# Kernel tuning notes

Measured on AMD Instinct MI355X. Metric: run time of the kernel, lower is better.

The kernel has to match this reference:

```python
import jax, jax.numpy as jnp
import numpy as np

N = 8192
IN_F = 256
OUT_F = 256
ALPHA = 0.2  # LeakyReLU negative slope
NEG_INF = -1e12


def setup_inputs() -> dict:
    key = jax.random.key(0)
    k1, k2, k3, k4, k5 = jax.random.split(key, 5)
    inp = jax.random.normal(k1, (N, IN_F), dtype=jnp.float32)
    adj = jax.random.randint(k2, (N, N), 0, 2, dtype=jnp.int32)
    # xavier_uniform with gain=1.414
    def xavier(k, shape, gain=1.414):
        fan_in, fan_out = shape[0], shape[1]
        bound = gain * np.sqrt(6.0 / (fan_in + fan_out))
        return jax.random.uniform(k, shape, jnp.float32, -bound, bound)
    W = xavier(k3, (IN_F, OUT_F))
    a = xavier(k4, (2 * OUT_F, 1))
    wtrans = xavier(k5, (2 * IN_F, OUT_F))
    return {"inp": inp, "adj": adj, "W": W, "a": a, "wtrans": wtrans}


def reference(inp, adj, W, a, wtrans):
    h = inp @ W                                  # [N, OUT_F]
    Wh1 = h @ a[:OUT_F, :]                       # [N, 1]
    Wh2 = h @ a[OUT_F:, :]                       # [N, 1]
    e = jax.nn.leaky_relu(Wh1 + Wh2.T, ALPHA)    # [N, N]
    mask = adj > 0
    attention = jax.nn.softmax(jnp.where(mask, e, NEG_INF), axis=1)
    negative_attention = -jax.nn.softmax(jnp.where(mask, -e, NEG_INF), axis=1)
    # dropout=0.0 / eval mode -> identity
    h_prime = attention @ inp                    # [N, IN_F]
    h_prime_negative = negative_attention @ inp  # [N, IN_F]
    h_prime_double = jnp.concatenate([h_prime, h_prime_negative], axis=1)
    new_h_prime = h_prime_double @ wtrans        # [N, OUT_F]
    return jax.nn.elu(new_h_prime)               # concat=True
```

## Files before the change

kernel.cpp:

```cpp
#include <hip/hip_runtime.h>
#include <stdint.h>

#define GN 8192

typedef float f32x4 __attribute__((ext_vector_type(4)));
typedef short s16x8 __attribute__((ext_vector_type(8)));
typedef unsigned short u16x8 __attribute__((ext_vector_type(8)));

__device__ __forceinline__ unsigned short f2bf(float f) {
    unsigned int u = __float_as_uint(f);
    u += 0x7FFFu + ((u >> 16) & 1u);
    return (unsigned short)(u >> 16);
}
__device__ __forceinline__ float bf2f(unsigned short h) {
    return __uint_as_float(((unsigned int)h) << 16);
}

__global__ void kA(const float* __restrict__ W, const float* __restrict__ a,
                   float* __restrict__ w1, float* __restrict__ w2) {
    int k = blockIdx.x, l = threadIdx.x;
    float s1 = 0.f, s2 = 0.f;
#pragma unroll
    for (int q = 0; q < 4; ++q) {
        int o = l + q * 64;
        float w = W[k * 256 + o];
        s1 += w * a[o];
        s2 += w * a[256 + o];
    }
#pragma unroll
    for (int off = 32; off; off >>= 1) {
        s1 += __shfl_xor(s1, off);
        s2 += __shfl_xor(s2, off);
    }
    if (l == 0) {
        w1[k] = s1;
        w2[k] = s2;
    }
}

__global__ void kA2(const float* __restrict__ wt, unsigned short* __restrict__ wtT) {
    int k = blockIdx.x;
    int o = threadIdx.x;
    wtT[(size_t)o * 512 + k] = f2bf(wt[(size_t)k * 256 + o]);
}

__global__ __launch_bounds__(256) void kB(const float* __restrict__ inp,
                                          const float* __restrict__ w1,
                                          const float* __restrict__ w2,
                                          float* __restrict__ s, float* __restrict__ t,
                                          unsigned short* __restrict__ inpT) {
    __shared__ unsigned short T[256][33];
    const int tid = threadIdx.x;
    const int r0 = blockIdx.x * 32;
    const int r = tid >> 3, cs = tid & 7;
    const float4* in4 = (const float4*)(inp + (size_t)(r0 + r) * 256 + cs * 32);
    const float4* w14 = (const float4*)(w1 + cs * 32);
    const float4* w24 = (const float4*)(w2 + cs * 32);
    float zs = 0.f, zt = 0.f;
#pragma unroll
    for (int q = 0; q < 8; ++q) {
        float4 v = in4[q];
        float4 a1 = w14[q];
        float4 a2 = w24[q];
        zs += v.x * a1.x + v.y * a1.y + v.z * a1.z + v.w * a1.w;
        zt += v.x * a2.x + v.y * a2.y + v.z * a2.z + v.w * a2.w;
        int c = cs * 32 + q * 4;
        T[c + 0][r] = f2bf(v.x);
        T[c + 1][r] = f2bf(v.y);
        T[c + 2][r] = f2bf(v.z);
        T[c + 3][r] = f2bf(v.w);
    }
#pragma unroll
    for (int off = 1; off < 8; off <<= 1) {
        zs += __shfl_xor(zs, off);
        zt += __shfl_xor(zt, off);
    }
    if (cs == 0) {
        s[r0 + r] = zs;
        t[r0 + r] = zt;
    }
    __syncthreads();
    unsigned short* dst = inpT + (size_t)tid * GN + r0;
    ushort4* d4 = (ushort4*)dst;
#pragma unroll
    for (int q = 0; q < 8; ++q) {
        ushort4 v;
        v.x = T[tid][q * 4 + 0];
        v.y = T[tid][q * 4 + 1];
        v.z = T[tid][q * 4 + 2];
        v.w = T[tid][q * 4 + 3];
        d4[q] = v;
    }
}

#define PROC(AM, TX, BP, BN)                  \
    {                                         \
        float e = sr + (TX);                  \
        float l = fmaxf(e, 0.2f * e);         \
        float p1 = (AM) ? __expf(l) : 0.f;    \
        float p2 = (AM) ? __expf(-l) : 0.f;   \
        unsigned short b1 = f2bf(p1);         \
        unsigned short b2 = f2bf(p2);         \
        zp += bf2f(b1);                       \
        zn += bf2f(b2);                       \
        BP = b1;                              \
        BN = b2;                              \
    }

__global__ __launch_bounds__(512, 2) void kC(const int* __restrict__ adj,
                                             const float* __restrict__ sv,
                                             const float* __restrict__ tv,
                                             const unsigned short* __restrict__ inpT,
                                             const unsigned short* __restrict__ wtT,
                                             float* __restrict__ out) {
    __shared__ unsigned short ptP[32 * 256];
    __shared__ unsigned short ptN[32 * 256];
    __shared__ unsigned short hdl[32 * 512];
    __shared__ float Zs[64];
    const int tid = threadIdx.x;
    const int lane = tid & 63, w = tid >> 6;
    const int rr = lane & 15, hi = lane >> 4;
    const int r = tid >> 4, c4 = tid & 15;
    const int i0 = blockIdx.x * 32;
    const float sr = sv[i0 + r];
    float zp = 0.f, zn = 0.f;
    f32x4 accP[2][2], accN[2][2];
#pragma unroll
    for (int m = 0; m < 2; ++m)
#pragma unroll
        for (int n = 0; n < 2; ++n) {
            accP[m][n] = (f32x4)(0.f);
            accN[m][n] = (f32x4)(0.f);
        }
    const int fb = w * 32;
    char* ldsP = (char*)ptP;
    char* ldsN = (char*)ptN;
    const int swz = (r & 7) << 4;
    const int wb0 = (r * 512 + c4 * 32) ^ swz;
    const int wb1 = (r * 512 + c4 * 32 + 16) ^ swz;
    const size_t arow = (size_t)(i0 + r) * GN + c4 * 16;
    const float* tb = tv + c4 * 16;

    int4 ca0 = *(const int4*)(adj + arow);
    int4 ca1 = *(const int4*)(adj + arow + 4);
    int4 ca2 = *(const int4*)(adj + arow + 8);
    int4 ca3 = *(const int4*)(adj + arow + 12);
    float4 tf0 = *(const float4*)(tb);
    float4 tf1 = *(const float4*)(tb + 4);
    float4 tf2 = *(const float4*)(tb + 8);
    float4 tf3 = *(const float4*)(tb + 12);

    for (int jc = 0; jc < 32; ++jc) {
        s16x8 bvr[16];
        const unsigned short* bcol = inpT + jc * 256 + hi * 8;
#pragma unroll
        for (int kc = 0; kc < 8; ++kc) {
            bvr[kc * 2 + 0] = *(const s16x8*)(bcol + (size_t)(fb + rr) * GN + kc * 32);
            bvr[kc * 2 + 1] = *(const s16x8*)(bcol + (size_t)(fb + 16 + rr) * GN + kc * 32);
        }
        u16x8 up0, up1, un0, un1;
        PROC(ca0.x, tf0.x, up0[0], un0[0]);
        PROC(ca0.y, tf0.y, up0[1], un0[1]);
        PROC(ca0.z, tf0.z, up0[2], un0[2]);
        PROC(ca0.w, tf0.w, up0[3], un0[3]);
        PROC(ca1.x, tf1.x, up0[4], un0[4]);
        PROC(ca1.y, tf1.y, up0[5], un0[5]);
        PROC(ca1.z, tf1.z, up0[6], un0[6]);
        PROC(ca1.w, tf1.w, up0[7], un0[7]);
        PROC(ca2.x, tf2.x, up1[0], un1[0]);
        PROC(ca2.y, tf2.y, up1[1], un1[1]);
        PROC(ca2.z, tf2.z, up1[2], un1[2]);
        PROC(ca2.w, tf2.w, up1[3], un1[3]);
        PROC(ca3.x, tf3.x, up1[4], un1[4]);
        PROC(ca3.y, tf3.y, up1[5], un1[5]);
        PROC(ca3.z, tf3.z, up1[6], un1[6]);
        PROC(ca3.w, tf3.w, up1[7], un1[7]);
        if (jc < 31) {
            const int* an = adj + arow + (jc + 1) * 256;
            ca0 = *(const int4*)(an);
            ca1 = *(const int4*)(an + 4);
            ca2 = *(const int4*)(an + 8);
            ca3 = *(const int4*)(an + 12);
            const float* tn = tb + (jc + 1) * 256;
            tf0 = *(const float4*)(tn);
            tf1 = *(const float4*)(tn + 4);
            tf2 = *(const float4*)(tn + 8);
            tf3 = *(const float4*)(tn + 12);
        }
        asm volatile("" ::: "memory");
        __builtin_amdgcn_s_barrier();
        asm volatile("" ::: "memory");
        *(u16x8*)(ldsP + wb0) = up0;
        *(u16x8*)(ldsP + wb1) = up1;
        *(u16x8*)(ldsN + wb0) = un0;
        *(u16x8*)(ldsN + wb1) = un1;
        asm volatile("s_waitcnt lgkmcnt(0)" ::: "memory");
        __builtin_amdgcn_s_barrier();
        asm volatile("" ::: "memory");
#pragma unroll
        for (int kc = 0; kc < 8; ++kc) {
            int rb0 = (rr * 512 + kc * 64 + hi * 16) ^ ((rr & 7) << 4);
            s16x8 aP0 = *(const s16x8*)(ldsP + rb0);
            s16x8 aP1 = *(const s16x8*)(ldsP + rb0 + 8192);
            s16x8 aN0 = *(const s16x8*)(ldsN + rb0);
            s16x8 aN1 = *(const s16x8*)(ldsN + rb0 + 8192);
            accP[0][0] = __builtin_amdgcn_mfma_f32_16x16x32_bf16(aP0, bvr[kc * 2 + 0], accP[0][0], 0, 0, 0);
            accP[1][0] = __builtin_amdgcn_mfma_f32_16x16x32_bf16(aP1, bvr[kc * 2 + 0], accP[1][0], 0, 0, 0);
            accN[0][0] = __builtin_amdgcn_mfma_f32_16x16x32_bf16(aN0, bvr[kc * 2 + 0], accN[0][0], 0, 0, 0);
            accN[1][0] = __builtin_amdgcn_mfma_f32_16x16x32_bf16(aN1, bvr[kc * 2 + 0], accN[1][0], 0, 0, 0);
            accP[0][1] = __builtin_amdgcn_mfma_f32_16x16x32_bf16(aP0, bvr[kc * 2 + 1], accP[0][1], 0, 0, 0);
            accP[1][1] = __builtin_amdgcn_mfma_f32_16x16x32_bf16(aP1, bvr[kc * 2 + 1], accP[1][1], 0, 0, 0);
            accN[0][1] = __builtin_amdgcn_mfma_f32_16x16x32_bf16(aN0, bvr[kc * 2 + 1], accN[0][1], 0, 0, 0);
            accN[1][1] = __builtin_amdgcn_mfma_f32_16x16x32_bf16(aN1, bvr[kc * 2 + 1], accN[1][1], 0, 0, 0);
        }
    }
#pragma unroll
    for (int off = 1; off < 16; off <<= 1) {
        zp += __shfl_xor(zp, off);
        zn += __shfl_xor(zn, off);
    }
    if (c4 == 0) {
        Zs[r] = zp;
        Zs[32 + r] = zn;
    }
    __syncthreads();
#pragma unroll
    for (int m = 0; m < 2; ++m)
#pragma unroll
        for (int reg = 0; reg < 4; ++reg) {
            int row = m * 16 + hi * 4 + reg;
            float izp = 1.f / Zs[row];
            float izn = 1.f / Zs[32 + row];
            int sw = (row & 7) << 4;
#pragma unroll
            for (int nt = 0; nt < 2; ++nt) {
                int col = fb + nt * 16 + rr;
                *(unsigned short*)((char*)hdl + ((row * 1024 + col * 2) ^ sw)) =
                    f2bf(accP[m][nt][reg] * izp);
                *(unsigned short*)((char*)hdl + ((row * 1024 + (col + 256) * 2) ^ sw)) =
                    f2bf(-accN[m][nt][reg] * izn);
            }
        }
    __syncthreads();
    f32x4 oc[2][2];
#pragma unroll
    for (int m = 0; m < 2; ++m)
#pragma unroll
        for (int nt = 0; nt < 2; ++nt) oc[m][nt] = (f32x4)(0.f);
    const int n0 = w * 32;
#pragma unroll
    for (int kc = 0; kc < 16; ++kc) {
        int rbs = (rr & 7) << 4;
        s16x8 a0 = *(const s16x8*)((char*)hdl + ((rr * 1024 + kc * 64 + hi * 16) ^ rbs));
        s16x8 a1 = *(const s16x8*)((char*)hdl + (((16 + rr) * 1024 + kc * 64 + hi * 16) ^ rbs));
#pragma unroll
        for (int nt = 0; nt < 2; ++nt) {
            s16x8 b = *(const s16x8*)(wtT + (size_t)(n0 + nt * 16 + rr) * 512 + kc * 32 + hi * 8);
            oc[0][nt] = __builtin_amdgcn_mfma_f32_16x16x32_bf16(a0, b, oc[0][nt], 0, 0, 0);
            oc[1][nt] = __builtin_amdgcn_mfma_f32_16x16x32_bf16(a1, b, oc[1][nt], 0, 0, 0);
        }
    }
#pragma unroll
    for (int m = 0; m < 2; ++m)
#pragma unroll
        for (int nt = 0; nt < 2; ++nt) {
            int col = n0 + nt * 16 + rr;
#pragma unroll
            for (int reg = 0; reg < 4; ++reg) {
                int row = i0 + m * 16 + hi * 4 + reg;
                float x = oc[m][nt][reg];
                out[(size_t)row * 256 + col] = x > 0.f ? x : __expf(x) - 1.f;
            }
        }
}

extern "C" void kernel_launch(void* const* d_in, const int* in_sizes, int n_in,
                              void* d_out, int out_size, void* d_ws, size_t ws_size,
                              hipStream_t stream) {
    const float* inp = (const float*)d_in[0];
    const int* adj = (const int*)d_in[1];
    const float* W = (const float*)d_in[2];
    const float* a = (const float*)d_in[3];
    const float* wt = (const float*)d_in[4];
    float* out = (float*)d_out;
    char* ws = (char*)d_ws;

    unsigned short* inpT = (unsigned short*)ws;
    float* s = (float*)(ws + (4 << 20));
    float* t = (float*)(ws + (4 << 20) + (1 << 15));
    float* w1 = (float*)(ws + (4 << 20) + (2 << 15));
    float* w2 = (float*)(ws + (4 << 20) + (2 << 15) + 4096);
    unsigned short* wtT = (unsigned short*)(ws + (4 << 20) + (2 << 15) + 8192);

    hipLaunchKernelGGL(kA, dim3(256), dim3(64), 0, stream, W, a, w1, w2);
    hipLaunchKernelGGL(kA2, dim3(512), dim3(256), 0, stream, wt, wtT);
    hipLaunchKernelGGL(kB, dim3(256), dim3(256), 0, stream, inp, w1, w2, s, t, inpT);
    hipLaunchKernelGGL(kC, dim3(256), dim3(512), 0, stream, adj, s, t, inpT, wtT, out);
}
```

Before: 474.3 us.

## Halve kC row tile to 16 rows, double grid, use exp2 and nontemporal adj loads

The main attention kernel now processes 16 rows per block instead of 32. That doubles the grid to 512 blocks, shrinks LDS use by sharing one buffer between the probability tiles and the h_prime tile, and raises occupancy to 4 blocks per CU. Logits are prescaled by log2(e) so the kernel can call exp2f, adjacency loads are marked nontemporal, and the wtrans transpose now goes through a coalesced shared-memory tile. The trade-off is that each block loads the inp B-operand for half as many rows, so global and L2 traffic for inpT doubles.

```diff
diff --git a/kernel.cpp b/kernel.cpp
--- a/kernel.cpp
+++ b/kernel.cpp
@@ -2,10 +2,12 @@
 #include <stdint.h>
 
 #define GN 8192
+#define LOG2E 1.4426950408889634f
 
 typedef float f32x4 __attribute__((ext_vector_type(4)));
 typedef short s16x8 __attribute__((ext_vector_type(8)));
 typedef unsigned short u16x8 __attribute__((ext_vector_type(8)));
+typedef int i32x4 __attribute__((ext_vector_type(4)));
 
 __device__ __forceinline__ unsigned short f2bf(float f) {
     unsigned int u = __float_as_uint(f);
@@ -33,15 +35,29 @@
         s2 += __shfl_xor(s2, off);
     }
     if (l == 0) {
-        w1[k] = s1;
-        w2[k] = s2;
-    }
-}
-
-__global__ void kA2(const float* __restrict__ wt, unsigned short* __restrict__ wtT) {
-    int k = blockIdx.x;
-    int o = threadIdx.x;
-    wtT[(size_t)o * 512 + k] = f2bf(wt[(size_t)k * 256 + o]);
+        w1[k] = s1 * LOG2E;
+        w2[k] = s2 * LOG2E;
+    }
+}
+
+__global__ __launch_bounds__(256) void kA2(const float* __restrict__ wt,
+                                           unsigned short* __restrict__ wtT) {
+    __shared__ unsigned short Tt[32][33];
+    const int bi = blockIdx.x;
+    const int bj = blockIdx.y;
+    const int ty = threadIdx.x >> 3, tx8 = threadIdx.x & 7;
+    float4 v = *(const float4*)(wt + (size_t)(bj * 32 + ty) * 256 + bi * 32 + tx8 * 4);
+    Tt[tx8 * 4 + 0][ty] = f2bf(v.x);
+    Tt[tx8 * 4 + 1][ty] = f2bf(v.y);
+    Tt[tx8 * 4 + 2][ty] = f2bf(v.z);
+    Tt[tx8 * 4 + 3][ty] = f2bf(v.w);
+    __syncthreads();
+    ushort4 o4;
+    o4.x = Tt[ty][tx8 * 4 + 0];
+    o4.y = Tt[ty][tx8 * 4 + 1];
+    o4.z = Tt[ty][tx8 * 4 + 2];
+    o4.w = Tt[ty][tx8 * 4 + 3];
+    *(ushort4*)(wtT + (size_t)(bi * 32 + ty) * 512 + bj * 32 + tx8 * 4) = o4;
 }
 
 __global__ __launch_bounds__(256) void kB(const float* __restrict__ inp,
@@ -93,62 +109,51 @@
     }
 }
 
-#define PROC(AM, TX, BP, BN)                  \
-    {                                         \
-        float e = sr + (TX);                  \
-        float l = fmaxf(e, 0.2f * e);         \
-        float p1 = (AM) ? __expf(l) : 0.f;    \
-        float p2 = (AM) ? __expf(-l) : 0.f;   \
-        unsigned short b1 = f2bf(p1);         \
-        unsigned short b2 = f2bf(p2);         \
-        zp += bf2f(b1);                       \
-        zn += bf2f(b2);                       \
-        BP = b1;                              \
-        BN = b2;                              \
-    }
-
-__global__ __launch_bounds__(512, 2) void kC(const int* __restrict__ adj,
+#define PROC(AM, TX, BP, BN)                   \
+    {                                          \
+        float e = sr + (TX);                   \
+        float l = fmaxf(e, 0.2f * e);          \
+        float p1 = (AM) ? exp2f(l) : 0.f;      \
+        float p2 = (AM) ? exp2f(-l) : 0.f;     \
+        unsigned short b1 = f2bf(p1);          \
+        unsigned short b2 = f2bf(p2);          \
+        zp += bf2f(b1);                        \
+        zn += bf2f(b2);                        \
+        BP = b1;                               \
+        BN = b2;                               \
+    }
+
+__global__ __launch_bounds__(512, 4) void kC(const int* __restrict__ adj,
                                              const float* __restrict__ sv,
                                              const float* __restrict__ tv,
                                              const unsigned short* __restrict__ inpT,
                                              const unsigned short* __restrict__ wtT,
                                              float* __restrict__ out) {
-    __shared__ unsigned short ptP[32 * 256];
-    __shared__ unsigned short ptN[32 * 256];
-    __shared__ unsigned short hdl[32 * 512];
-    __shared__ float Zs[64];
+    __shared__ __align__(16) char smem[16384];
+    __shared__ float Zs[32];
+    char* ldsP = smem;
+    char* ldsN = smem + 8192;
     const int tid = threadIdx.x;
     const int lane = tid & 63, w = tid >> 6;
     const int rr = lane & 15, hi = lane >> 4;
-    const int r = tid >> 4, c4 = tid & 15;
-    const int i0 = blockIdx.x * 32;
+    const int r = tid >> 5, c8 = tid & 31;
+    const int i0 = blockIdx.x * 16;
     const float sr = sv[i0 + r];
     float zp = 0.f, zn = 0.f;
-    f32x4 accP[2][2], accN[2][2];
-#pragma unroll
-    for (int m = 0; m < 2; ++m)
-#pragma unroll
-        for (int n = 0; n < 2; ++n) {
-            accP[m][n] = (f32x4)(0.f);
-            accN[m][n] = (f32x4)(0.f);
-        }
+    f32x4 accP[2], accN[2];
+    accP[0] = (f32x4)(0.f);
+    accP[1] = (f32x4)(0.f);
+    accN[0] = (f32x4)(0.f);
+    accN[1] = (f32x4)(0.f);
     const int fb = w * 32;
-    char* ldsP = (char*)ptP;
-    char* ldsN = (char*)ptN;
-    const int swz = (r & 7) << 4;
-    const int wb0 = (r * 512 + c4 * 32) ^ swz;
-    const int wb1 = (r * 512 + c4 * 32 + 16) ^ swz;
-    const size_t arow = (size_t)(i0 + r) * GN + c4 * 16;
-    const float* tb = tv + c4 * 16;
-
-    int4 ca0 = *(const int4*)(adj + arow);
-    int4 ca1 = *(const int4*)(adj + arow + 4);
-    int4 ca2 = *(const int4*)(adj + arow + 8);
-    int4 ca3 = *(const int4*)(adj + arow + 12);
+    const int wb = (r * 512 + c8 * 16) ^ ((r & 7) << 4);
+    const size_t arow = (size_t)(i0 + r) * GN + c8 * 8;
+    const float* tb = tv + c8 * 8;
+
+    i32x4 ca0 = __builtin_nontemporal_load((const i32x4*)(adj + arow));
+    i32x4 ca1 = __builtin_nontemporal_load((const i32x4*)(adj + arow + 4));
     float4 tf0 = *(const float4*)(tb);
     float4 tf1 = *(const float4*)(tb + 4);
-    float4 tf2 = *(const float4*)(tb + 8);
-    float4 tf3 = *(const float4*)(tb + 12);
 
     for (int jc = 0; jc < 32; ++jc) {
         s16x8 bvr[16];
@@ -158,120 +163,92 @@
             bvr[kc * 2 + 0] = *(const s16x8*)(bcol + (size_t)(fb + rr) * GN + kc * 32);
             bvr[kc * 2 + 1] = *(const s16x8*)(bcol + (size_t)(fb + 16 + rr) * GN + kc * 32);
         }
-        u16x8 up0, up1, un0, un1;
-        PROC(ca0.x, tf0.x, up0[0], un0[0]);
-        PROC(ca0.y, tf0.y, up0[1], un0[1]);
-        PROC(ca0.z, tf0.z, up0[2], un0[2]);
-        PROC(ca0.w, tf0.w, up0[3], un0[3]);
-        PROC(ca1.x, tf1.x, up0[4], un0[4]);
-        PROC(ca1.y, tf1.y, up0[5], un0[5]);
-        PROC(ca1.z, tf1.z, up0[6], un0[6]);
-        PROC(ca1.w, tf1.w, up0[7], un0[7]);
-        PROC(ca2.x, tf2.x, up1[0], un1[0]);
-        PROC(ca2.y, tf2.y, up1[1], un1[1]);
-        PROC(ca2.z, tf2.z, up1[2], un1[2]);
-        PROC(ca2.w, tf2.w, up1[3], un1[3]);
-        PROC(ca3.x, tf3.x, up1[4], un1[4]);
-        PROC(ca3.y, tf3.y, up1[5], un1[5]);
-        PROC(ca3.z, tf3.z, up1[6], un1[6]);
-        PROC(ca3.w, tf3.w, up1[7], un1[7]);
+        u16x8 up, un;
+        PROC(ca0.x, tf0.x, up[0], un[0]);
+        PROC(ca0.y, tf0.y, up[1], un[1]);
+        PROC(ca0.z, tf0.z, up[2], un[2]);
+        PROC(ca0.w, tf0.w, up[3], un[3]);
+        PROC(ca1.x, tf1.x, up[4], un[4]);
+        PROC(ca1.y, tf1.y, up[5], un[5]);
+        PROC(ca1.z, tf1.z, up[6], un[6]);
+        PROC(ca1.w, tf1.w, up[7], un[7]);
         if (jc < 31) {
             const int* an = adj + arow + (jc + 1) * 256;
-            ca0 = *(const int4*)(an);
-            ca1 = *(const int4*)(an + 4);
-            ca2 = *(const int4*)(an + 8);
-            ca3 = *(const int4*)(an + 12);
+            ca0 = __builtin_nontemporal_load((const i32x4*)(an));
+            ca1 = __builtin_nontemporal_load((const i32x4*)(an + 4));
             const float* tn = tb + (jc + 1) * 256;
             tf0 = *(const float4*)(tn);
             tf1 = *(const float4*)(tn + 4);
-            tf2 = *(const float4*)(tn + 8);
-            tf3 = *(const float4*)(tn + 12);
         }
         asm volatile("" ::: "memory");
         __builtin_amdgcn_s_barrier();
         asm volatile("" ::: "memory");
-        *(u16x8*)(ldsP + wb0) = up0;
-        *(u16x8*)(ldsP + wb1) = up1;
-        *(u16x8*)(ldsN + wb0) = un0;
-        *(u16x8*)(ldsN + wb1) = un1;
+        *(u16x8*)(ldsP + wb) = up;
+        *(u16x8*)(ldsN + wb) = un;
         asm volatile("s_waitcnt lgkmcnt(0)" ::: "memory");
         __builtin_amdgcn_s_barrier();
         asm volatile("" ::: "memory");
 #pragma unroll
         for (int kc = 0; kc < 8; ++kc) {
-            int rb0 = (rr * 512 + kc * 64 + hi * 16) ^ ((rr & 7) << 4);
-            s16x8 aP0 = *(const s16x8*)(ldsP + rb0);
-            s16x8 aP1 = *(const s16x8*)(ldsP + rb0 + 8192);
-            s16x8 aN0 = *(const s16x8*)(ldsN + rb0);
-            s16x8 aN1 = *(const s16x8*)(ldsN + rb0 + 8192);
-            accP[0][0] = __builtin_amdgcn_mfma_f32_16x16x32_bf16(aP0, bvr[kc * 2 + 0], accP[0][0], 0, 0, 0);
-            accP[1][0] = __builtin_amdgcn_mfma_f32_16x16x32_bf16(aP1, bvr[kc * 2 + 0], accP[1][0], 0, 0, 0);
-            accN[0][0] = __builtin_amdgcn_mfma_f32_16x16x32_bf16(aN0, bvr[kc * 2 + 0], accN[0][0], 0, 0, 0);
-            accN[1][0] = __builtin_amdgcn_mfma_f32_16x16x32_bf16(aN1, bvr[kc * 2 + 0], accN[1][0], 0, 0, 0);
-            accP[0][1] = __builtin_amdgcn_mfma_f32_16x16x32_bf16(aP0, bvr[kc * 2 + 1], accP[0][1], 0, 0, 0);
-            accP[1][1] = __builtin_amdgcn_mfma_f32_16x16x32_bf16(aP1, bvr[kc * 2 + 1], accP[1][1], 0, 0, 0);
-            accN[0][1] = __builtin_amdgcn_mfma_f32_16x16x32_bf16(aN0, bvr[kc * 2 + 1], accN[0][1], 0, 0, 0);
-            accN[1][1] = __builtin_amdgcn_mfma_f32_16x16x32_bf16(aN1, bvr[kc * 2 + 1], accN[1][1], 0, 0, 0);
-        }
-    }
-#pragma unroll
-    for (int off = 1; off < 16; off <<= 1) {
+            int rb = (rr * 512 + kc * 64 + hi * 16) ^ ((rr & 7) << 4);
+            s16x8 aP = *(const s16x8*)(ldsP + rb);
+            s16x8 aN = *(const s16x8*)(ldsN + rb);
+            accP[0] = __builtin_amdgcn_mfma_f32_16x16x32_bf16(aP, bvr[kc * 2 + 0], accP[0], 0, 0, 0);
+            accP[1] = __builtin_amdgcn_mfma_f32_16x16x32_bf16(aP, bvr[kc * 2 + 1], accP[1], 0, 0, 0);
+            accN[0] = __builtin_amdgcn_mfma_f32_16x16x32_bf16(aN, bvr[kc * 2 + 0], accN[0], 0, 0, 0);
+            accN[1] = __builtin_amdgcn_mfma_f32_16x16x32_bf16(aN, bvr[kc * 2 + 1], accN[1], 0, 0, 0);
+        }
+    }
+#pragma unroll
+    for (int off = 1; off < 32; off <<= 1) {
         zp += __shfl_xor(zp, off);
         zn += __shfl_xor(zn, off);
     }
-    if (c4 == 0) {
+    if ((tid & 31) == 0) {
         Zs[r] = zp;
-        Zs[32 + r] = zn;
-    }
-    __syncthreads();
-#pragma unroll
-    for (int m = 0; m < 2; ++m)
+        Zs[16 + r] = zn;
+    }
+    __syncthreads();
+    char* hdl = smem;
+#pragma unroll
+    for (int reg = 0; reg < 4; ++reg) {
+        int row = hi * 4 + reg;
+        float izp = 1.f / Zs[row];
+        float izn = 1.f / Zs[16 + row];
+        int sw = (row & 7) << 4;
+#pragma unroll
+        for (int nt = 0; nt < 2; ++nt) {
+            int col = fb + nt * 16 + rr;
+            *(unsigned short*)(hdl + ((row * 1024 + col * 2) ^ sw)) =
+                f2bf(accP[nt][reg] * izp);
+            *(unsigned short*)(hdl + ((row * 1024 + (col + 256) * 2) ^ sw)) =
+                f2bf(-accN[nt][reg] * izn);
+        }
+    }
+    __syncthreads();
+    f32x4 oc[2];
+    oc[0] = (f32x4)(0.f);
+    oc[1] = (f32x4)(0.f);
+#pragma unroll
+    for (int kc = 0; kc < 16; ++kc) {
+        int rb = (rr * 1024 + kc * 64 + hi * 16) ^ ((rr & 7) << 4);
+        s16x8 av = *(const s16x8*)(hdl + rb);
+#pragma unroll
+        for (int nt = 0; nt < 2; ++nt) {
+            s16x8 b = *(const s16x8*)(wtT + (size_t)(fb + nt * 16 + rr) * 512 + kc * 32 + hi * 8);
+            oc[nt] = __builtin_amdgcn_mfma_f32_16x16x32_bf16(av, b, oc[nt], 0, 0, 0);
+        }
+    }
+#pragma unroll
+    for (int nt = 0; nt < 2; ++nt) {
+        int col = fb + nt * 16 + rr;
 #pragma unroll
         for (int reg = 0; reg < 4; ++reg) {
-            int row = m * 16 + hi * 4 + reg;
-            float izp = 1.f / Zs[row];
-            float izn = 1.f / Zs[32 + row];
-            int sw = (row & 7) << 4;
-#pragma unroll
-            for (int nt = 0; nt < 2; ++nt) {
-                int col = fb + nt * 16 + rr;
-                *(unsigned short*)((char*)hdl + ((row * 1024 + col * 2) ^ sw)) =
-                    f2bf(accP[m][nt][reg] * izp);
-                *(unsigned short*)((char*)hdl + ((row * 1024 + (col + 256) * 2) ^ sw)) =
-                    f2bf(-accN[m][nt][reg] * izn);
-            }
-        }
-    __syncthreads();
-    f32x4 oc[2][2];
-#pragma unroll
-    for (int m = 0; m < 2; ++m)
-#pragma unroll
-        for (int nt = 0; nt < 2; ++nt) oc[m][nt] = (f32x4)(0.f);
-    const int n0 = w * 32;
-#pragma unroll
-    for (int kc = 0; kc < 16; ++kc) {
-        int rbs = (rr & 7) << 4;
-        s16x8 a0 = *(const s16x8*)((char*)hdl + ((rr * 1024 + kc * 64 + hi * 16) ^ rbs));
-        s16x8 a1 = *(const s16x8*)((char*)hdl + (((16 + rr) * 1024 + kc * 64 + hi * 16) ^ rbs));
-#pragma unroll
-        for (int nt = 0; nt < 2; ++nt) {
-            s16x8 b = *(const s16x8*)(wtT + (size_t)(n0 + nt * 16 + rr) * 512 + kc * 32 + hi * 8);
-            oc[0][nt] = __builtin_amdgcn_mfma_f32_16x16x32_bf16(a0, b, oc[0][nt], 0, 0, 0);
-            oc[1][nt] = __builtin_amdgcn_mfma_f32_16x16x32_bf16(a1, b, oc[1][nt], 0, 0, 0);
-        }
-    }
-#pragma unroll
-    for (int m = 0; m < 2; ++m)
-#pragma unroll
-        for (int nt = 0; nt < 2; ++nt) {
-            int col = n0 + nt * 16 + rr;
-#pragma unroll
-            for (int reg = 0; reg < 4; ++reg) {
-                int row = i0 + m * 16 + hi * 4 + reg;
-                float x = oc[m][nt][reg];
-                out[(size_t)row * 256 + col] = x > 0.f ? x : __expf(x) - 1.f;
-            }
-        }
+            int row = i0 + hi * 4 + reg;
+            float x = oc[nt][reg];
+            out[(size_t)row * 256 + col] = x > 0.f ? x : __expf(x) - 1.f;
+        }
+    }
 }
 
 extern "C" void kernel_launch(void* const* d_in, const int* in_sizes, int n_in,
@@ -293,7 +270,7 @@
     unsigned short* wtT = (unsigned short*)(ws + (4 << 20) + (2 << 15) + 8192);
 
     hipLaunchKernelGGL(kA, dim3(256), dim3(64), 0, stream, W, a, w1, w2);
-    hipLaunchKernelGGL(kA2, dim3(512), dim3(256), 0, stream, wt, wtT);
+    hipLaunchKernelGGL(kA2, dim3(8, 16), dim3(256), 0, stream, wt, wtT);
     hipLaunchKernelGGL(kB, dim3(256), dim3(256), 0, stream, inp, w1, w2, s, t, inpT);
-    hipLaunchKernelGGL(kC, dim3(256), dim3(512), 0, stream, adj, s, t, inpT, wtT, out);
-}
+    hipLaunchKernelGGL(kC, dim3(512), dim3(512), 0, stream, adj, s, t, inpT, wtT, out);
+}
```

Result: slower. 591.8 us (+24.8%).
